# Kernel tuning notes

Hardware: AMD Instinct MI355X
Metric: run time of the kernel (lower is better)

## Reference

```python
import jax, jax.numpy as jnp
import numpy as np

B, C_IN, C_OUT, H, W = 32, 3, 32, 256, 256


def setup_inputs() -> dict:
    key = jax.random.key(0)
    ks = jax.random.split(key, 10)
    x1 = jax.random.normal(ks[0], (B, C_IN, H, W), dtype=jnp.float32)
    x2 = jax.random.normal(ks[1], (B, C_IN, H, W), dtype=jnp.float32)
    scale = 1.0 / np.sqrt(C_IN)
    Wq = jax.random.normal(ks[2], (C_OUT, C_IN), dtype=jnp.float32) * scale
    bq = jax.random.normal(ks[3], (C_OUT,), dtype=jnp.float32) * 0.01
    Wk = jax.random.normal(ks[4], (C_OUT, C_IN), dtype=jnp.float32) * scale
    bk = jax.random.normal(ks[5], (C_OUT,), dtype=jnp.float32) * 0.01
    Wv = jax.random.normal(ks[6], (C_OUT, C_IN), dtype=jnp.float32) * scale
    bv = jax.random.normal(ks[7], (C_OUT,), dtype=jnp.float32) * 0.01
    Wa = jax.random.normal(ks[8], (C_OUT, C_IN), dtype=jnp.float32) * scale
    ba = jax.random.normal(ks[9], (C_OUT,), dtype=jnp.float32) * 0.01
    return {"x1": x1, "x2": x2, "Wq": Wq, "bq": bq, "Wk": Wk, "bk": bk,
            "Wv": Wv, "bv": bv, "Wa": Wa, "ba": ba}


def _proj(x, Wmat, b):
    # 1x1 conv == per-pixel channel matmul: [B,Cin,H,W] -> [B,Cout,H,W]
    return jnp.einsum('bchw,oc->bohw', x, Wmat) + b[None, :, None, None]


def reference(x1, x2, Wq, bq, Wk, bk, Wv, bv, Wa, ba):
    q = _proj(x1, Wq, bq)   # [B,32,H,W]
    k = _proj(x2, Wk, bk)   # [B,32,H,W]
    v = _proj(x2, Wv, bv)   # [B,32,H,W]
    a = _proj(x2, Wa, ba)   # [B,32,H,W] (H==W so it adds to scores)
    inv_scale = 1.0 / q.shape[-1]
    # q @ k^T over last two dims: [B,32,H,W] @ [B,32,W,H] -> [B,32,H,H]
    scores = jnp.einsum('bohw,bogw->bohg', q, k) * inv_scale + a
    att = jax.nn.softmax(scores, axis=-1)
    # att @ v: [B,32,H,H] @ [B,32,H,W] -> [B,32,H,W]
    return jnp.einsum('bohg,bogw->bohw', att, v)
```

## Files before the change

kernel.cpp:

```cpp
#include <hip/hip_runtime.h>

typedef __bf16 bf16x8 __attribute__((ext_vector_type(8)));
typedef __bf16 bf16x4 __attribute__((ext_vector_type(4)));
typedef float  f32x4  __attribute__((ext_vector_type(4)));

#define HW   256
#define HW2  65536

__global__ __launch_bounds__(512, 2) void attn_kernel(
    const float* __restrict__ x1, const float* __restrict__ x2,
    const float* __restrict__ Wq, const float* __restrict__ bq,
    const float* __restrict__ Wk, const float* __restrict__ bk,
    const float* __restrict__ Wv, const float* __restrict__ bv,
    const float* __restrict__ Wa, const float* __restrict__ ba,
    float* __restrict__ out)
{
    __shared__ __align__(16) __bf16 sKV[64 * 264];
    __shared__ __align__(16) __bf16 sVT[256 * 72];
    __shared__ __align__(16) __bf16 sP[128 * 264];
    __shared__ float sRow[128];

    const int tid  = threadIdx.x;
    const int wid  = tid >> 6;
    const int lane = tid & 63;
    const int quad = lane >> 4;
    const int c    = lane & 15;

    const int blk  = blockIdx.x;
    const int pair = blk >> 1;
    const int ht   = blk & 1;
    const int b    = pair >> 5;
    const int o    = pair & 31;
    const int h0   = ht * 128;

    const float wq0 = Wq[o*3+0], wq1 = Wq[o*3+1], wq2 = Wq[o*3+2], bqv = bq[o];
    const float wk0 = Wk[o*3+0], wk1 = Wk[o*3+1], wk2 = Wk[o*3+2], bkv = bk[o];
    const float wv0 = Wv[o*3+0], wv1 = Wv[o*3+1], wv2 = Wv[o*3+2], bvv = bv[o];
    const float wa0 = Wa[o*3+0], wa1 = Wa[o*3+1], wa2 = Wa[o*3+2], bav = ba[o];
    const float inv = 1.0f / 256.0f;

    const float* x1b = x1 + b * 3 * HW2;
    const float* x2b = x2 + b * 3 * HW2;

    bf16x8 qf[8];
    {
        const int hq = h0 + 16*wid + c;
        const float* r0 = x1b + 0*HW2 + hq*HW;
        const float* r1 = x1b + 1*HW2 + hq*HW;
        const float* r2 = x1b + 2*HW2 + hq*HW;
#pragma unroll
        for (int kt = 0; kt < 8; ++kt) {
            const int wc = 32*kt + 8*quad;
            float4 a0 = *(const float4*)(r0 + wc), a1 = *(const float4*)(r0 + wc + 4);
            float4 b0 = *(const float4*)(r1 + wc), b1 = *(const float4*)(r1 + wc + 4);
            float4 c0 = *(const float4*)(r2 + wc), c1 = *(const float4*)(r2 + wc + 4);
            bf16x8 q;
            q[0] = (__bf16)((wq0*a0.x + wq1*b0.x + wq2*c0.x + bqv) * inv);
            q[1] = (__bf16)((wq0*a0.y + wq1*b0.y + wq2*c0.y + bqv) * inv);
            q[2] = (__bf16)((wq0*a0.z + wq1*b0.z + wq2*c0.z + bqv) * inv);
            q[3] = (__bf16)((wq0*a0.w + wq1*b0.w + wq2*c0.w + bqv) * inv);
            q[4] = (__bf16)((wq0*a1.x + wq1*b1.x + wq2*c1.x + bqv) * inv);
            q[5] = (__bf16)((wq0*a1.y + wq1*b1.y + wq2*c1.y + bqv) * inv);
            q[6] = (__bf16)((wq0*a1.z + wq1*b1.z + wq2*c1.z + bqv) * inv);
            q[7] = (__bf16)((wq0*a1.w + wq1*b1.w + wq2*c1.w + bqv) * inv);
            qf[kt] = q;
        }
    }

    f32x4 acc[16];
#pragma unroll
    for (int g0i = 0; g0i < 4; ++g0i) {
        const int g0 = g0i * 64;
        __syncthreads();
#pragma unroll
        for (int i = 0; i < 8; ++i) {
            const int s   = i*512 + tid;
            const int row = s >> 6;
            const int c4  = (s & 63) * 4;
            const int g   = g0 + row;
            float4 u0 = *(const float4*)(x2b + 0*HW2 + g*HW + c4);
            float4 u1 = *(const float4*)(x2b + 1*HW2 + g*HW + c4);
            float4 u2 = *(const float4*)(x2b + 2*HW2 + g*HW + c4);
            bf16x4 kv;
            kv[0] = (__bf16)(wk0*u0.x + wk1*u1.x + wk2*u2.x + bkv);
            kv[1] = (__bf16)(wk0*u0.y + wk1*u1.y + wk2*u2.y + bkv);
            kv[2] = (__bf16)(wk0*u0.z + wk1*u1.z + wk2*u2.z + bkv);
            kv[3] = (__bf16)(wk0*u0.w + wk1*u1.w + wk2*u2.w + bkv);
            *(bf16x4*)(&sKV[row*264 + c4]) = kv;
        }
        __syncthreads();
#pragma unroll
        for (int ag = 0; ag < 4; ++ag) {
            const int ai   = g0i*4 + ag;
            const int gcol = g0 + 16*ag + c;
            f32x4 a;
#pragma unroll
            for (int r = 0; r < 4; ++r) {
                const int hh = h0 + 16*wid + 4*quad + r;
                a[r] = wa0 * x2b[0*HW2 + hh*HW + gcol]
                     + wa1 * x2b[1*HW2 + hh*HW + gcol]
                     + wa2 * x2b[2*HW2 + hh*HW + gcol] + bav;
            }
#pragma unroll
            for (int kt = 0; kt < 8; ++kt) {
                bf16x8 bf = *(const bf16x8*)(&sKV[(16*ag + c)*264 + 32*kt + 8*quad]);
                a = __builtin_amdgcn_mfma_f32_16x16x32_bf16(qf[kt], bf, a, 0, 0, 0);
            }
            acc[ai] = a;
        }
    }

    float lrow[4];
#pragma unroll
    for (int r = 0; r < 4; ++r) {
        float m = acc[0][r];
#pragma unroll
        for (int t = 1; t < 16; ++t) m = fmaxf(m, acc[t][r]);
#pragma unroll
        for (int d = 8; d >= 1; d >>= 1) m = fmaxf(m, __shfl_xor(m, d, 64));
        float l = 0.0f;
#pragma unroll
        for (int t = 0; t < 16; ++t) {
            float e = __expf(acc[t][r] - m);
            acc[t][r] = e;
            l += e;
        }
#pragma unroll
        for (int d = 8; d >= 1; d >>= 1) l += __shfl_xor(l, d, 64);
        lrow[r] = l;
    }
    if (c == 0) {
#pragma unroll
        for (int r = 0; r < 4; ++r) sRow[16*wid + 4*quad + r] = lrow[r];
    }
#pragma unroll
    for (int t = 0; t < 16; ++t) {
#pragma unroll
        for (int r = 0; r < 4; ++r) {
            sP[(16*wid + 4*quad + r)*264 + 16*t + c] = (__bf16)acc[t][r];
        }
    }

    f32x4 oacc[16];
#pragma unroll
    for (int t = 0; t < 16; ++t) oacc[t] = (f32x4){0.f, 0.f, 0.f, 0.f};

    for (int g0i = 0; g0i < 4; ++g0i) {
        const int g0 = g0i * 64;
        __syncthreads();
        {
            const int w  = tid & 255;
            const int gs = (tid >> 8) * 32;
#pragma unroll
            for (int i = 0; i < 8; ++i) {
                const int gl = gs + i*4;
                const int g  = g0 + gl;
                bf16x4 pk;
#pragma unroll
                for (int j = 0; j < 4; ++j) {
                    float u0 = x2b[0*HW2 + (g+j)*HW + w];
                    float u1 = x2b[1*HW2 + (g+j)*HW + w];
                    float u2 = x2b[2*HW2 + (g+j)*HW + w];
                    pk[j] = (__bf16)(wv0*u0 + wv1*u1 + wv2*u2 + bvv);
                }
                *(bf16x4*)(&sVT[w*72 + gl]) = pk;
            }
        }
        __syncthreads();
        bf16x8 pf0 = *(const bf16x8*)(&sP[(16*wid + c)*264 + g0 +  0 + 8*quad]);
        bf16x8 pf1 = *(const bf16x8*)(&sP[(16*wid + c)*264 + g0 + 32 + 8*quad]);
#pragma unroll
        for (int wt = 0; wt < 16; ++wt) {
            bf16x8 vf0 = *(const bf16x8*)(&sVT[(16*wt + c)*72 +  0 + 8*quad]);
            oacc[wt] = __builtin_amdgcn_mfma_f32_16x16x32_bf16(vf0, pf0, oacc[wt], 0, 0, 0);
            bf16x8 vf1 = *(const bf16x8*)(&sVT[(16*wt + c)*72 + 32 + 8*quad]);
            oacc[wt] = __builtin_amdgcn_mfma_f32_16x16x32_bf16(vf1, pf1, oacc[wt], 0, 0, 0);
        }
    }

    const float rinv = 1.0f / sRow[16*wid + c];
    float* outp = out + (size_t)pair * HW2 + (size_t)(h0 + 16*wid + c) * HW;
#pragma unroll
    for (int wt = 0; wt < 16; ++wt) {
#pragma unroll
        for (int r = 0; r < 4; ++r) {
            outp[16*wt + 4*quad + r] = oacc[wt][r] * rinv;
        }
    }
}

extern "C" void kernel_launch(void* const* d_in, const int* in_sizes, int n_in,
                              void* d_out, int out_size, void* d_ws, size_t ws_size,
                              hipStream_t stream) {
    const float* x1 = (const float*)d_in[0];
    const float* x2 = (const float*)d_in[1];
    const float* Wq = (const float*)d_in[2];
    const float* bq = (const float*)d_in[3];
    const float* Wk = (const float*)d_in[4];
    const float* bk = (const float*)d_in[5];
    const float* Wv = (const float*)d_in[6];
    const float* bv = (const float*)d_in[7];
    const float* Wa = (const float*)d_in[8];
    const float* ba = (const float*)d_in[9];
    float* out = (float*)d_out;

    attn_kernel<<<dim3(2048), dim3(512), 0, stream>>>(
        x1, x2, Wq, bq, Wk, bk, Wv, bv, Wa, ba, out);
}
```

Measured before the change: 669.8 us.

## Switch to online softmax fused with PV accumulation to shrink shared memory

```diff
diff --git a/kernel.cpp b/kernel.cpp
--- a/kernel.cpp
+++ b/kernel.cpp
@@ -7,7 +7,7 @@
 #define HW   256
 #define HW2  65536
 
-__global__ __launch_bounds__(512, 2) void attn_kernel(
+__global__ __launch_bounds__(512, 4) void attn_kernel(
     const float* __restrict__ x1, const float* __restrict__ x2,
     const float* __restrict__ Wq, const float* __restrict__ bq,
     const float* __restrict__ Wk, const float* __restrict__ bk,
@@ -15,9 +15,9 @@
     const float* __restrict__ Wa, const float* __restrict__ ba,
     float* __restrict__ out)
 {
-    __shared__ __align__(16) __bf16 sKV[64 * 264];
-    __shared__ __align__(16) __bf16 sVT[256 * 72];
-    __shared__ __align__(16) __bf16 sP[128 * 264];
+    __shared__ __align__(16) __bf16 sU[256 * 72];
+    __shared__ __align__(16) __bf16 sPc[128 * 72];
+    __shared__ float sFac[128];
     __shared__ float sRow[128];
 
     const int tid  = threadIdx.x;
@@ -67,10 +67,28 @@
         }
     }
 
-    f32x4 acc[16];
-#pragma unroll
+    f32x4 oacc[16];
+#pragma unroll
+    for (int t = 0; t < 16; ++t) oacc[t] = (f32x4){0.f, 0.f, 0.f, 0.f};
+    float m_run[4] = {-1e30f, -1e30f, -1e30f, -1e30f};
+    float l_run[4] = {0.f, 0.f, 0.f, 0.f};
+
     for (int g0i = 0; g0i < 4; ++g0i) {
         const int g0 = g0i * 64;
+
+        float aini[16];
+#pragma unroll
+        for (int ag = 0; ag < 4; ++ag) {
+            const int gcol = g0 + 16*ag + c;
+#pragma unroll
+            for (int r = 0; r < 4; ++r) {
+                const int hh = h0 + 16*wid + 4*quad + r;
+                aini[4*ag + r] = wa0 * x2b[0*HW2 + hh*HW + gcol]
+                               + wa1 * x2b[1*HW2 + hh*HW + gcol]
+                               + wa2 * x2b[2*HW2 + hh*HW + gcol] + bav;
+            }
+        }
+
         __syncthreads();
 #pragma unroll
         for (int i = 0; i < 8; ++i) {
@@ -86,68 +104,59 @@
             kv[1] = (__bf16)(wk0*u0.y + wk1*u1.y + wk2*u2.y + bkv);
             kv[2] = (__bf16)(wk0*u0.z + wk1*u1.z + wk2*u2.z + bkv);
             kv[3] = (__bf16)(wk0*u0.w + wk1*u1.w + wk2*u2.w + bkv);
-            *(bf16x4*)(&sKV[row*264 + c4]) = kv;
-        }
-        __syncthreads();
+            *(bf16x4*)(&sU[row*264 + c4]) = kv;
+        }
+        __syncthreads();
+
+        f32x4 accc[4];
 #pragma unroll
         for (int ag = 0; ag < 4; ++ag) {
-            const int ai   = g0i*4 + ag;
-            const int gcol = g0 + 16*ag + c;
             f32x4 a;
 #pragma unroll
+            for (int r = 0; r < 4; ++r) a[r] = aini[4*ag + r];
+#pragma unroll
+            for (int kt = 0; kt < 8; ++kt) {
+                bf16x8 bf = *(const bf16x8*)(&sU[(16*ag + c)*264 + 32*kt + 8*quad]);
+                a = __builtin_amdgcn_mfma_f32_16x16x32_bf16(qf[kt], bf, a, 0, 0, 0);
+            }
+            accc[ag] = a;
+        }
+
+        float fac[4];
+#pragma unroll
+        for (int r = 0; r < 4; ++r) {
+            float mc = fmaxf(fmaxf(accc[0][r], accc[1][r]),
+                             fmaxf(accc[2][r], accc[3][r]));
+#pragma unroll
+            for (int d = 8; d >= 1; d >>= 1) mc = fmaxf(mc, __shfl_xor(mc, d, 64));
+            const float mn = fmaxf(m_run[r], mc);
+            const float f  = __expf(m_run[r] - mn);
+            m_run[r] = mn;
+            fac[r] = f;
+            float l = 0.0f;
+#pragma unroll
+            for (int ag = 0; ag < 4; ++ag) {
+                float e = __expf(accc[ag][r] - mn);
+                accc[ag][r] = e;
+                l += e;
+            }
+#pragma unroll
+            for (int d = 8; d >= 1; d >>= 1) l += __shfl_xor(l, d, 64);
+            l_run[r] = l_run[r]*f + l;
+        }
+        if (c == 0) {
+#pragma unroll
+            for (int r = 0; r < 4; ++r) sFac[16*wid + 4*quad + r] = fac[r];
+        }
+#pragma unroll
+        for (int ag = 0; ag < 4; ++ag) {
+#pragma unroll
             for (int r = 0; r < 4; ++r) {
-                const int hh = h0 + 16*wid + 4*quad + r;
-                a[r] = wa0 * x2b[0*HW2 + hh*HW + gcol]
-                     + wa1 * x2b[1*HW2 + hh*HW + gcol]
-                     + wa2 * x2b[2*HW2 + hh*HW + gcol] + bav;
-            }
-#pragma unroll
-            for (int kt = 0; kt < 8; ++kt) {
-                bf16x8 bf = *(const bf16x8*)(&sKV[(16*ag + c)*264 + 32*kt + 8*quad]);
-                a = __builtin_amdgcn_mfma_f32_16x16x32_bf16(qf[kt], bf, a, 0, 0, 0);
-            }
-            acc[ai] = a;
-        }
-    }
-
-    float lrow[4];
-#pragma unroll
-    for (int r = 0; r < 4; ++r) {
-        float m = acc[0][r];
-#pragma unroll
-        for (int t = 1; t < 16; ++t) m = fmaxf(m, acc[t][r]);
-#pragma unroll
-        for (int d = 8; d >= 1; d >>= 1) m = fmaxf(m, __shfl_xor(m, d, 64));
-        float l = 0.0f;
-#pragma unroll
-        for (int t = 0; t < 16; ++t) {
-            float e = __expf(acc[t][r] - m);
-            acc[t][r] = e;
-            l += e;
-        }
-#pragma unroll
-        for (int d = 8; d >= 1; d >>= 1) l += __shfl_xor(l, d, 64);
-        lrow[r] = l;
-    }
-    if (c == 0) {
-#pragma unroll
-        for (int r = 0; r < 4; ++r) sRow[16*wid + 4*quad + r] = lrow[r];
-    }
-#pragma unroll
-    for (int t = 0; t < 16; ++t) {
-#pragma unroll
-        for (int r = 0; r < 4; ++r) {
-            sP[(16*wid + 4*quad + r)*264 + 16*t + c] = (__bf16)acc[t][r];
-        }
-    }
-
-    f32x4 oacc[16];
-#pragma unroll
-    for (int t = 0; t < 16; ++t) oacc[t] = (f32x4){0.f, 0.f, 0.f, 0.f};
-
-    for (int g0i = 0; g0i < 4; ++g0i) {
-        const int g0 = g0i * 64;
-        __syncthreads();
+                sPc[(16*wid + 4*quad + r)*72 + 16*ag + c] = (__bf16)accc[ag][r];
+            }
+        }
+        __syncthreads();
+
         {
             const int w  = tid & 255;
             const int gs = (tid >> 8) * 32;
@@ -163,21 +172,31 @@
                     float u2 = x2b[2*HW2 + (g+j)*HW + w];
                     pk[j] = (__bf16)(wv0*u0 + wv1*u1 + wv2*u2 + bvv);
                 }
-                *(bf16x4*)(&sVT[w*72 + gl]) = pk;
-            }
-        }
-        __syncthreads();
-        bf16x8 pf0 = *(const bf16x8*)(&sP[(16*wid + c)*264 + g0 +  0 + 8*quad]);
-        bf16x8 pf1 = *(const bf16x8*)(&sP[(16*wid + c)*264 + g0 + 32 + 8*quad]);
+                *(bf16x4*)(&sU[w*72 + gl]) = pk;
+            }
+        }
+        __syncthreads();
+
+        const float fc = sFac[16*wid + c];
+        bf16x8 pf0 = *(const bf16x8*)(&sPc[(16*wid + c)*72 +  0 + 8*quad]);
+        bf16x8 pf1 = *(const bf16x8*)(&sPc[(16*wid + c)*72 + 32 + 8*quad]);
 #pragma unroll
         for (int wt = 0; wt < 16; ++wt) {
-            bf16x8 vf0 = *(const bf16x8*)(&sVT[(16*wt + c)*72 +  0 + 8*quad]);
-            oacc[wt] = __builtin_amdgcn_mfma_f32_16x16x32_bf16(vf0, pf0, oacc[wt], 0, 0, 0);
-            bf16x8 vf1 = *(const bf16x8*)(&sVT[(16*wt + c)*72 + 32 + 8*quad]);
-            oacc[wt] = __builtin_amdgcn_mfma_f32_16x16x32_bf16(vf1, pf1, oacc[wt], 0, 0, 0);
-        }
-    }
-
+            f32x4 oa = oacc[wt];
+            oa[0] *= fc; oa[1] *= fc; oa[2] *= fc; oa[3] *= fc;
+            bf16x8 vf0 = *(const bf16x8*)(&sU[(16*wt + c)*72 +  0 + 8*quad]);
+            oa = __builtin_amdgcn_mfma_f32_16x16x32_bf16(vf0, pf0, oa, 0, 0, 0);
+            bf16x8 vf1 = *(const bf16x8*)(&sU[(16*wt + c)*72 + 32 + 8*quad]);
+            oa = __builtin_amdgcn_mfma_f32_16x16x32_bf16(vf1, pf1, oa, 0, 0, 0);
+            oacc[wt] = oa;
+        }
+    }
+
+    if (c == 0) {
+#pragma unroll
+        for (int r = 0; r < 4; ++r) sRow[16*wid + 4*quad + r] = l_run[r];
+    }
+    __syncthreads();
     const float rinv = 1.0f / sRow[16*wid + c];
     float* outp = out + (size_t)pair * HW2 + (size_t)(h0 + 16*wid + c) * HW;
 #pragma unroll
```

Result: slower. 1.284 ms (+91.7%).
